# Optimization experiments

Hardware: AMD Instinct MI355X
Metric: run time of the kernel (lower is better)

The kernel has to match this reference:

```python
import jax, jax.numpy as jnp
import numpy as np
import math

D_MODEL = 1024
NUM_HEADS = 16
HEAD_DIM = D_MODEL // NUM_HEADS
THETA = 10000.0
B, S = 2, 2048


def _rope(x, positions, theta):
    # x: (b, h, s, d); positions: (s,) int
    d = x.shape[-1]
    inv_freq = theta ** (-jnp.arange(0, d, 2, dtype=jnp.float32) / d)  # (d/2,)
    ang = positions.astype(jnp.float32)[:, None] * inv_freq[None, :]   # (s, d/2)
    cos, sin = jnp.cos(ang), jnp.sin(ang)
    x1 = x[..., ::2]
    x2 = x[..., 1::2]
    r1 = x1 * cos - x2 * sin
    r2 = x1 * sin + x2 * cos
    # interleave back to (..., d)
    return jnp.stack([r1, r2], axis=-1).reshape(x.shape)


def setup_inputs() -> dict:
    key = jax.random.key(0)
    ks = jax.random.split(key, 5)
    std = math.sqrt(2.0 / (D_MODEL + D_MODEL))
    return {
        "x": jax.random.normal(ks[0], (B, S, D_MODEL), dtype=jnp.float32),
        "token_positions": jnp.arange(S, dtype=jnp.int32),
        "Wq": jax.random.normal(ks[1], (D_MODEL, D_MODEL), dtype=jnp.float32) * std,
        "Wk": jax.random.normal(ks[2], (D_MODEL, D_MODEL), dtype=jnp.float32) * std,
        "Wv": jax.random.normal(ks[3], (D_MODEL, D_MODEL), dtype=jnp.float32) * std,
        "Wo": jax.random.normal(ks[4], (D_MODEL, D_MODEL), dtype=jnp.float32) * std,
    }


def reference(x, token_positions, Wq, Wk, Wv, Wo):
    b, s, _ = x.shape
    def split_heads(t):
        return t.reshape(b, s, NUM_HEADS, HEAD_DIM).transpose(0, 2, 1, 3)  # (b,h,s,d)
    Q = split_heads(x @ Wq.T)
    K = split_heads(x @ Wk.T)
    V = split_heads(x @ Wv.T)
    Q = _rope(Q, token_positions, THETA)
    K = _rope(K, token_positions, THETA)
    scores = jnp.einsum("bhqd,bhkd->bhqk", Q, K) / math.sqrt(HEAD_DIM)
    causal = jnp.tril(jnp.ones((s, s), dtype=bool))
    scores = jnp.where(causal, scores, -jnp.inf)
    attn = jax.nn.softmax(scores, axis=-1)
    out = jnp.einsum("bhqk,bhkd->bhqd", attn, V)
    out = out.transpose(0, 2, 1, 3).reshape(b, s, D_MODEL)
    return out @ Wo.T
```

## Files before the change

kernel.cpp:

```cpp
#include <hip/hip_runtime.h>
#include <math.h>

typedef unsigned short u16;
typedef unsigned int   u32;
typedef __attribute__((ext_vector_type(8))) short bf16x8;
typedef __attribute__((ext_vector_type(4))) float floatx4;
typedef __attribute__((ext_vector_type(4))) _Float16 halfx4;
typedef __attribute__((ext_vector_type(2))) unsigned int uintx2;

#define SEQ 2048
#define DM  1024
#define NH  16
#define DH  64
#define MM  4096
#define QSCALE 0.18033688011112042f

__device__ __forceinline__ u16 f2bf(float f) {
    u32 u = __builtin_bit_cast(u32, f);
    u += 0x7fffu + ((u >> 16) & 1u);
    return (u16)(u >> 16);
}

__device__ __forceinline__ void async16(const void* g, void* l) {
    __builtin_amdgcn_global_load_lds(
        (const __attribute__((address_space(1))) void*)g,
        (__attribute__((address_space(3))) void*)l, 16, 0, 0);
}

__global__ __launch_bounds__(256) void prep_kernel(const float* __restrict__ x,
                                                   const float* __restrict__ w0,
                                                   const float* __restrict__ w1,
                                                   const float* __restrict__ w2,
                                                   const float* __restrict__ w3,
                                                   u16* __restrict__ Xsh,
                                                   u16* __restrict__ Wsh,
                                                   const int* __restrict__ pos,
                                                   float2* __restrict__ tab) {
    const int bid = blockIdx.x, cb = blockIdx.y, tid = threadIdx.x;

    int lin = bid * 16 + cb;
    if (lin < 256) {
        int i = lin * 256 + tid;
        int p = i >> 5, d2 = i & 31;
        float freq = __expf(-(float)d2 * (9.2103403719761836f / 32.0f));
        float sv, cv;
        sincosf((float)pos[p] * freq, &sv, &cv);
        tab[i] = make_float2(cv, sv);
    }

    const float* src; u16* dst; int row0;
    if (bid < 64) { src = x; dst = Xsh; row0 = bid * 64; }
    else {
        int wi = (bid - 64) >> 4;
        src = (wi == 0) ? w0 : (wi == 1) ? w1 : (wi == 2) ? w2 : w3;
        dst = Wsh + (size_t)wi * DM * DM;
        row0 = ((bid - 64) & 15) * 64;
    }
    __shared__ __align__(16) u16 t[64 * 64];
#pragma unroll
    for (int rep = 0; rep < 4; ++rep) {
        int f = rep * 256 + tid;
        int r = f >> 4, c4 = f & 15;
        float4 v = *(const float4*)&src[(size_t)(row0 + r) * DM + cb * 64 + c4 * 4];
        uint2 pk;
        pk.x = (u32)f2bf(v.x) | ((u32)f2bf(v.y) << 16);
        pk.y = (u32)f2bf(v.z) | ((u32)f2bf(v.w) << 16);
        int ch = (c4 >> 1) ^ (r & 7);
        *(uint2*)&t[r * 64 + ch * 8 + (c4 & 1) * 4] = pk;
    }
    __syncthreads();
#pragma unroll
    for (int rep = 0; rep < 2; ++rep) {
        int s = rep * 256 + tid;
        int tile = s >> 6, l = s & 63;
        int mt = tile >> 1, kt = tile & 1, lm = l & 15, quad = l >> 4;
        int m = mt * 16 + lm;
        uint4 v = *(const uint4*)&t[m * 64 + ((kt * 4 + quad) ^ (m & 7)) * 8];
        size_t rowblk = (size_t)(row0 >> 4) + mt;
        size_t ktile  = cb * 2 + kt;
        *(uint4*)&dst[(rowblk * 32 + ktile) * 512 + l * 8] = v;
    }
}

template<int NZ, bool OUTF32>
__global__ __launch_bounds__(256, 2) void gemm_f(const u16* __restrict__ Ash,
                                                 const u16* __restrict__ Wbase,
                                                 u16* __restrict__ outbf,
                                                 float* __restrict__ outf,
                                                 _Float16* __restrict__ vtout,
                                                 const float2* __restrict__ ropetab) {
    const int m0 = blockIdx.x * 64, n0 = blockIdx.y * 128;
    const int tid = threadIdx.x, lane = tid & 63, w = tid >> 6;
    const int lm = lane & 15, quad = lane >> 4;
    const int rb0 = m0 >> 4;
    const int cb0 = n0 >> 4;

    __shared__ __align__(16) u16 lsA[2][4 * 512];
    __shared__ __align__(16) u16 lsB[2][NZ * 8 * 512];

    const u16* aSrc = Ash + ((size_t)(rb0 + w) * 32) * 512 + lane * 8;
    constexpr int NPW = NZ * 2;
    const u16* bSrc[NPW];
#pragma unroll
    for (int j = 0; j < NPW; ++j) {
        int p = w * NPW + j, z = p >> 3, cb8 = p & 7;
        bSrc[j] = Wbase + (size_t)z * (DM * DM)
                + ((size_t)(cb0 + cb8) * 32) * 512 + lane * 8;
    }

    auto stage = [&](int buf, int it) {
        async16(aSrc + (size_t)it * 512, &lsA[buf][w * 512 + lane * 8]);
#pragma unroll
        for (int j = 0; j < NPW; ++j)
            async16(bSrc[j] + (size_t)it * 512,
                    &lsB[buf][(w * NPW + j) * 512 + lane * 8]);
    };

    floatx4 acc[NZ][4][2];
    const floatx4 z4 = {0.f, 0.f, 0.f, 0.f};
#pragma unroll
    for (int z = 0; z < NZ; ++z)
#pragma unroll
        for (int mt = 0; mt < 4; ++mt)
#pragma unroll
            for (int nt = 0; nt < 2; ++nt) acc[z][mt][nt] = z4;

    stage(0, 0);
    __syncthreads();

#pragma unroll 2
    for (int it = 0; it < 32; ++it) {
        if (it < 31) stage((it + 1) & 1, it + 1);
        const u16* La = &lsA[it & 1][0];
        const u16* Lb = &lsB[it & 1][0];
        bf16x8 a[4], b[NZ][2];
#pragma unroll
        for (int mt = 0; mt < 4; ++mt)
            a[mt] = *(const bf16x8*)&La[mt * 512 + lane * 8];
#pragma unroll
        for (int z = 0; z < NZ; ++z)
#pragma unroll
            for (int nt = 0; nt < 2; ++nt)
                b[z][nt] = *(const bf16x8*)&Lb[(z * 8 + w * 2 + nt) * 512 + lane * 8];
#pragma unroll
        for (int z = 0; z < NZ; ++z)
#pragma unroll
            for (int mt = 0; mt < 4; ++mt)
#pragma unroll
                for (int nt = 0; nt < 2; ++nt)
                    acc[z][mt][nt] = __builtin_amdgcn_mfma_f32_16x16x32_bf16(
                        a[mt], b[z][nt], acc[z][mt][nt], 0, 0, 0);
        __syncthreads();
    }

#pragma unroll
    for (int z = 0; z < NZ; ++z) {
        if (!OUTF32 && NZ == 3 && z == 2) {
#pragma unroll
            for (int mt = 0; mt < 4; ++mt) {
                int row = m0 + mt * 16 + quad * 4;
                int b = row >> 11, s = row & (SEQ - 1);
#pragma unroll
                for (int nt = 0; nt < 2; ++nt) {
                    int col = n0 + w * 32 + nt * 16 + lm;
                    uint2 pk;
                    pk.x = __builtin_bit_cast(u32, __builtin_amdgcn_cvt_pkrtz(acc[z][mt][nt][0], acc[z][mt][nt][1]));
                    pk.y = __builtin_bit_cast(u32, __builtin_amdgcn_cvt_pkrtz(acc[z][mt][nt][2], acc[z][mt][nt][3]));
                    *(uint2*)&vtout[((size_t)b * NH * DH + (size_t)col) * SEQ + s] = pk;
                }
            }
            continue;
        }
        const bool rope = !OUTF32;
        const float osc = (!OUTF32 && z == 0) ? QSCALE : 1.0f;
#pragma unroll
        for (int mt = 0; mt < 4; ++mt)
#pragma unroll
            for (int r = 0; r < 4; ++r) {
                int row = m0 + mt * 16 + quad * 4 + r;
#pragma unroll
                for (int nt = 0; nt < 2; ++nt) {
                    int col = n0 + w * 32 + nt * 16 + lm;
                    float v  = acc[z][mt][nt][r];
                    if (rope) {
                        float pv = __shfl_xor(v, 1);
                        float2 cs = ropetab[(row & (SEQ - 1)) * 32 + ((col & 63) >> 1)];
                        v = (lm & 1) ? fmaf(pv, cs.y, v * cs.x) : fmaf(v, cs.x, -pv * cs.y);
                    }
                    v *= osc;
                    if (OUTF32) {
                        outf[(size_t)row * DM + col] = v;
                    } else {
                        float hv = __shfl_xor(v, 1);
                        if (!(lm & 1)) {
                            u32 pk = (u32)f2bf(v) | ((u32)f2bf(hv) << 16);
                            *(u32*)&outbf[(size_t)z * ((size_t)MM * DM) + (size_t)row * DM + col] = pk;
                        }
                    }
                }
            }
    }
}

__global__ __launch_bounds__(256, 2) void attn_kernel(const u16* __restrict__ Q,
                                                      const u16* __restrict__ K,
                                                      const _Float16* __restrict__ Vt,
                                                      u16* __restrict__ AO) {
    const int u  = blockIdx.x;
    const int qt = (u < 256) ? (15 - (u >> 5)) : ((u >> 5) - 8);
    const int bh = u & 31;
    const int b  = bh >> 4, h = bh & 15;
    const int q0 = qt * 128;
    const int tid = threadIdx.x, w = tid >> 6, lane = tid & 63;
    const int lm = lane & 15, quad = lane >> 4;

    __shared__ __align__(16) u16      lsK[2][128 * 64];
    __shared__ __align__(16) _Float16 lsV[2][64 * 128];

    bf16x8 qb[2][2];
#pragma unroll
    for (int qi = 0; qi < 2; ++qi)
#pragma unroll
        for (int ks = 0; ks < 2; ++ks)
            qb[qi][ks] = *(const bf16x8*)
                &Q[(size_t)(b * SEQ + q0 + w * 32 + qi * 16 + lm) * DM + h * DH + ks * 32 + quad * 8];

    const floatx4 z4 = {0.f, 0.f, 0.f, 0.f};
    floatx4 o[2][4];
#pragma unroll
    for (int qi = 0; qi < 2; ++qi)
#pragma unroll
        for (int dt = 0; dt < 4; ++dt) o[qi][dt] = z4;
    float lsum[2] = {0.f, 0.f};

    auto stageKV = [&](int buf, int kt) {
#pragma unroll
        for (int rep = 0; rep < 4; ++rep) {
            int f = rep * 256 + tid;
            int krow = f >> 3, kcb = (f & 7) ^ (krow & 7);
            async16(&K[(size_t)(b * SEQ + kt * 128 + krow) * DM + h * DH + kcb * 8],
                    &lsK[buf][f * 8]);
            int d = f >> 4, gbs = (f & 15) ^ ((d >> 1) & 7);
            async16(&Vt[(size_t)(bh * DH + d) * SEQ + kt * 128 + gbs * 8],
                    &lsV[buf][f * 8]);
        }
    };

    stageKV(0, 0);
    for (int kt = 0; kt <= qt; ++kt) {
        __syncthreads();
        if (kt < qt) stageKV((kt + 1) & 1, kt + 1);
        const u16*      Lk = lsK[kt & 1];
        const _Float16* Lv = lsV[kt & 1];

        floatx4 s4[2][8];
#pragma unroll
        for (int qi = 0; qi < 2; ++qi)
#pragma unroll
            for (int st = 0; st < 8; ++st) s4[qi][st] = z4;
#pragma unroll
        for (int ks = 0; ks < 2; ++ks) {
            const int cbl = ((ks * 4 + quad) ^ (lm & 7)) * 8;
#pragma unroll
            for (int st = 0; st < 8; ++st) {
                bf16x8 ka = *(const bf16x8*)&Lk[(st * 16 + lm) * 64 + cbl];
#pragma unroll
                for (int qi = 0; qi < 2; ++qi)
                    s4[qi][st] = __builtin_amdgcn_mfma_f32_16x16x32_bf16(ka, qb[qi][ks], s4[qi][st], 0, 0, 0);
            }
        }

        const bool diag = (kt == qt);
#pragma unroll
        for (int st = 0; st < 8; ++st) {
            halfx4 pb2[2];
#pragma unroll
            for (int qi = 0; qi < 2; ++qi) {
#pragma unroll
                for (int r = 0; r < 4; ++r) {
                    float v = s4[qi][st][r];
                    if (diag) {
                        int keyloc = st * 16 + quad * 4 + r;
                        if (keyloc > w * 32 + qi * 16 + lm) v = -1e30f;
                    }
                    v = exp2f(v);
                    lsum[qi] += v;
                    s4[qi][st][r] = v;
                }
                uintx2 pk2;
                pk2.x = __builtin_bit_cast(u32, __builtin_amdgcn_cvt_pkrtz(s4[qi][st][0], s4[qi][st][1]));
                pk2.y = __builtin_bit_cast(u32, __builtin_amdgcn_cvt_pkrtz(s4[qi][st][2], s4[qi][st][3]));
                pb2[qi] = __builtin_bit_cast(halfx4, pk2);
            }
#pragma unroll
            for (int dt = 0; dt < 4; ++dt) {
                int drow = dt * 16 + lm;
                int sbs = (st * 2 + (quad >> 1)) ^ ((drow >> 1) & 7);
                halfx4 va = *(const halfx4*)&Lv[drow * 128 + sbs * 8 + (quad & 1) * 4];
#pragma unroll
                for (int qi = 0; qi < 2; ++qi)
                    o[qi][dt] = __builtin_amdgcn_mfma_f32_16x16x16f16(va, pb2[qi], o[qi][dt], 0, 0, 0);
            }
        }
    }

    float rl[2];
#pragma unroll
    for (int qi = 0; qi < 2; ++qi) {
        lsum[qi] += __shfl_xor(lsum[qi], 16);
        lsum[qi] += __shfl_xor(lsum[qi], 32);
        rl[qi] = 1.0f / lsum[qi];
    }

    __syncthreads();
    u16* eb = (u16*)&lsK[0][0];
#pragma unroll
    for (int qi = 0; qi < 2; ++qi) {
        const int q = w * 32 + qi * 16 + lm;
#pragma unroll
        for (int dt = 0; dt < 4; ++dt) {
            uint2 pk;
            pk.x = (u32)f2bf(o[qi][dt][0] * rl[qi]) | ((u32)f2bf(o[qi][dt][1] * rl[qi]) << 16);
            pk.y = (u32)f2bf(o[qi][dt][2] * rl[qi]) | ((u32)f2bf(o[qi][dt][3] * rl[qi]) << 16);
            int ch = (dt * 2 + (quad >> 1)) ^ (lm & 7);
            *(uint2*)&eb[q * 64 + ch * 8 + (quad & 1) * 4] = pk;
        }
    }
    __syncthreads();
    const size_t rowblk0 = (size_t)((b * SEQ + q0) >> 4);
#pragma unroll
    for (int rbi = 0; rbi < 2; ++rbi) {
#pragma unroll
        for (int kt = 0; kt < 2; ++kt) {
            uint4 v = *(const uint4*)&eb[((w * 2 + rbi) * 16 + lm) * 64 + ((kt * 4 + quad) ^ (lm & 7)) * 8];
            *(uint4*)&AO[((rowblk0 + w * 2 + rbi) * 32 + (h * 2 + kt)) * 512 + lane * 8] = v;
        }
    }
}

extern "C" void kernel_launch(void* const* d_in, const int* in_sizes, int n_in,
                              void* d_out, int out_size, void* d_ws, size_t ws_size,
                              hipStream_t stream) {
    const float* x   = (const float*)d_in[0];
    const int*   pos = (const int*)d_in[1];
    float* out = (float*)d_out;

    u16* ws = (u16*)d_ws;
    const size_t MD = (size_t)MM * DM;
    const size_t DD = (size_t)DM * DM;
    u16* Xsh = ws;
    u16* Wsh = ws + MD;
    u16* Qbf = ws + MD + 4 * DD;
    u16* Kbf = Qbf + MD;
    u16* VtB = Kbf + MD;
    float2* ropetab = (float2*)(VtB + MD);
    _Float16* Vt = (_Float16*)VtB;
    u16* AOsh = Xsh;

    prep_kernel<<<dim3(128, 16), 256, 0, stream>>>(
        x, (const float*)d_in[2], (const float*)d_in[3], (const float*)d_in[4],
        (const float*)d_in[5], Xsh, Wsh, pos, ropetab);

    gemm_f<3, false><<<dim3(64, 8), 256, 0, stream>>>(
        Xsh, Wsh, Qbf, nullptr, Vt, ropetab);

    attn_kernel<<<dim3(512), 256, 0, stream>>>(Qbf, Kbf, Vt, AOsh);

    gemm_f<1, true><<<dim3(64, 8), 256, 0, stream>>>(
        AOsh, Wsh + 3 * DD, nullptr, out, nullptr, ropetab);
}
```

Measured before the change: 187.3 us.

## Store V in MFMA fragment order, halve KV tile, compute row sums via MFMA

The QKV projection now writes V in a chunked layout that matches the attention MFMA operand fragments, so V tiles load into LDS with contiguous copies and no swizzle. The attention loop moves to 64-key tiles with half-size LDS buffers and raises the occupancy target in launch bounds from 2 to 4 blocks. K is staged directly in fragment order. The softmax denominator is produced by an extra MFMA against a ones vector instead of scalar adds and cross-lane shuffles. This trades more loop iterations and barriers, plus one extra MFMA per step, for higher occupancy, simpler addressing and fewer VALU instructions.

```diff
diff --git a/kernel.cpp b/kernel.cpp
--- a/kernel.cpp
+++ b/kernel.cpp
@@ -158,15 +158,19 @@
         if (!OUTF32 && NZ == 3 && z == 2) {
 #pragma unroll
             for (int mt = 0; mt < 4; ++mt) {
-                int row = m0 + mt * 16 + quad * 4;
-                int b = row >> 11, s = row & (SEQ - 1);
+                int row = m0 + mt * 16;
+                int b = row >> 11;
+                int sblk = (row & (SEQ - 1)) >> 4;
 #pragma unroll
                 for (int nt = 0; nt < 2; ++nt) {
-                    int col = n0 + w * 32 + nt * 16 + lm;
+                    int col = n0 + w * 32 + nt * 16;
+                    int h = col >> 6;
+                    int dblk = (col & 63) >> 4;
+                    size_t chunk = ((size_t)(b * NH + h) * 128 + sblk) * 4 + dblk;
                     uint2 pk;
                     pk.x = __builtin_bit_cast(u32, __builtin_amdgcn_cvt_pkrtz(acc[z][mt][nt][0], acc[z][mt][nt][1]));
                     pk.y = __builtin_bit_cast(u32, __builtin_amdgcn_cvt_pkrtz(acc[z][mt][nt][2], acc[z][mt][nt][3]));
-                    *(uint2*)&vtout[((size_t)b * NH * DH + (size_t)col) * SEQ + s] = pk;
+                    *(uint2*)&vtout[chunk * 256 + lane * 4] = pk;
                 }
             }
             continue;
@@ -202,9 +206,9 @@
     }
 }
 
-__global__ __launch_bounds__(256, 2) void attn_kernel(const u16* __restrict__ Q,
+__global__ __launch_bounds__(256, 4) void attn_kernel(const u16* __restrict__ Q,
                                                       const u16* __restrict__ K,
-                                                      const _Float16* __restrict__ Vt,
+                                                      const _Float16* __restrict__ Vf,
                                                       u16* __restrict__ AO) {
     const int u  = blockIdx.x;
     const int qt = (u < 256) ? (15 - (u >> 5)) : ((u >> 5) - 8);
@@ -214,8 +218,8 @@
     const int tid = threadIdx.x, w = tid >> 6, lane = tid & 63;
     const int lm = lane & 15, quad = lane >> 4;
 
-    __shared__ __align__(16) u16      lsK[2][128 * 64];
-    __shared__ __align__(16) _Float16 lsV[2][64 * 128];
+    __shared__ __align__(16) u16      lsK[2][8 * 512];
+    __shared__ __align__(16) _Float16 lsV[2][16 * 256];
 
     bf16x8 qb[2][2];
 #pragma unroll
@@ -227,65 +231,70 @@
 
     const floatx4 z4 = {0.f, 0.f, 0.f, 0.f};
     floatx4 o[2][4];
-#pragma unroll
-    for (int qi = 0; qi < 2; ++qi)
+    floatx4 o5[2];
+#pragma unroll
+    for (int qi = 0; qi < 2; ++qi) {
 #pragma unroll
         for (int dt = 0; dt < 4; ++dt) o[qi][dt] = z4;
-    float lsum[2] = {0.f, 0.f};
+        o5[qi] = z4;
+    }
+
+    const u16* Kb = K + (size_t)(b * SEQ) * DM + h * DH + (size_t)lm * DM + quad * 8;
+    const _Float16* Vb = Vf + (size_t)bh * (128 * 4 * 256);
 
     auto stageKV = [&](int buf, int kt) {
 #pragma unroll
-        for (int rep = 0; rep < 4; ++rep) {
-            int f = rep * 256 + tid;
-            int krow = f >> 3, kcb = (f & 7) ^ (krow & 7);
-            async16(&K[(size_t)(b * SEQ + kt * 128 + krow) * DM + h * DH + kcb * 8],
-                    &lsK[buf][f * 8]);
-            int d = f >> 4, gbs = (f & 15) ^ ((d >> 1) & 7);
-            async16(&Vt[(size_t)(bh * DH + d) * SEQ + kt * 128 + gbs * 8],
-                    &lsV[buf][f * 8]);
+        for (int j = 0; j < 2; ++j) {
+            int c = w * 2 + j;
+            async16(Kb + (size_t)(kt * 64 + (c >> 1) * 16) * DM + (c & 1) * 32,
+                    &lsK[buf][c * 512 + lane * 8]);
+        }
+#pragma unroll
+        for (int p = 0; p < 2; ++p) {
+            int off = p * 2048 + w * 512 + lane * 8;
+            async16(Vb + (size_t)kt * 4096 + off, &lsV[buf][off]);
         }
     };
 
     stageKV(0, 0);
-    for (int kt = 0; kt <= qt; ++kt) {
+    const int nkt = 2 * qt + 2;
+    const halfx4 ones = {(_Float16)1.f, (_Float16)1.f, (_Float16)1.f, (_Float16)1.f};
+
+    for (int kt = 0; kt < nkt; ++kt) {
         __syncthreads();
-        if (kt < qt) stageKV((kt + 1) & 1, kt + 1);
+        if (kt + 1 < nkt) stageKV((kt + 1) & 1, kt + 1);
         const u16*      Lk = lsK[kt & 1];
         const _Float16* Lv = lsV[kt & 1];
 
-        floatx4 s4[2][8];
+        floatx4 s4[2][4];
 #pragma unroll
         for (int qi = 0; qi < 2; ++qi)
 #pragma unroll
-            for (int st = 0; st < 8; ++st) s4[qi][st] = z4;
-#pragma unroll
-        for (int ks = 0; ks < 2; ++ks) {
-            const int cbl = ((ks * 4 + quad) ^ (lm & 7)) * 8;
-#pragma unroll
-            for (int st = 0; st < 8; ++st) {
-                bf16x8 ka = *(const bf16x8*)&Lk[(st * 16 + lm) * 64 + cbl];
+            for (int st = 0; st < 4; ++st) s4[qi][st] = z4;
+#pragma unroll
+        for (int ks = 0; ks < 2; ++ks)
+#pragma unroll
+            for (int st = 0; st < 4; ++st) {
+                bf16x8 ka = *(const bf16x8*)&Lk[(st * 2 + ks) * 512 + lane * 8];
 #pragma unroll
                 for (int qi = 0; qi < 2; ++qi)
                     s4[qi][st] = __builtin_amdgcn_mfma_f32_16x16x32_bf16(ka, qb[qi][ks], s4[qi][st], 0, 0, 0);
             }
-        }
-
-        const bool diag = (kt == qt);
-#pragma unroll
-        for (int st = 0; st < 8; ++st) {
+
+        const int rel = kt - 2 * qt;
+#pragma unroll
+        for (int st = 0; st < 4; ++st) {
             halfx4 pb2[2];
 #pragma unroll
             for (int qi = 0; qi < 2; ++qi) {
 #pragma unroll
                 for (int r = 0; r < 4; ++r) {
                     float v = s4[qi][st][r];
-                    if (diag) {
-                        int keyloc = st * 16 + quad * 4 + r;
+                    if (rel >= 0) {
+                        int keyloc = rel * 64 + st * 16 + quad * 4 + r;
                         if (keyloc > w * 32 + qi * 16 + lm) v = -1e30f;
                     }
-                    v = exp2f(v);
-                    lsum[qi] += v;
-                    s4[qi][st][r] = v;
+                    s4[qi][st][r] = exp2f(v);
                 }
                 uintx2 pk2;
                 pk2.x = __builtin_bit_cast(u32, __builtin_amdgcn_cvt_pkrtz(s4[qi][st][0], s4[qi][st][1]));
@@ -294,23 +303,18 @@
             }
 #pragma unroll
             for (int dt = 0; dt < 4; ++dt) {
-                int drow = dt * 16 + lm;
-                int sbs = (st * 2 + (quad >> 1)) ^ ((drow >> 1) & 7);
-                halfx4 va = *(const halfx4*)&Lv[drow * 128 + sbs * 8 + (quad & 1) * 4];
+                halfx4 va = *(const halfx4*)&Lv[(st * 4 + dt) * 256 + lane * 4];
 #pragma unroll
                 for (int qi = 0; qi < 2; ++qi)
                     o[qi][dt] = __builtin_amdgcn_mfma_f32_16x16x16f16(va, pb2[qi], o[qi][dt], 0, 0, 0);
             }
-        }
-    }
-
-    float rl[2];
-#pragma unroll
-    for (int qi = 0; qi < 2; ++qi) {
-        lsum[qi] += __shfl_xor(lsum[qi], 16);
-        lsum[qi] += __shfl_xor(lsum[qi], 32);
-        rl[qi] = 1.0f / lsum[qi];
-    }
+#pragma unroll
+            for (int qi = 0; qi < 2; ++qi)
+                o5[qi] = __builtin_amdgcn_mfma_f32_16x16x16f16(ones, pb2[qi], o5[qi], 0, 0, 0);
+        }
+    }
+
+    float rl[2] = {1.0f / o5[0][0], 1.0f / o5[1][0]};
 
     __syncthreads();
     u16* eb = (u16*)&lsK[0][0];
```

After: 207.0 us. 10.5% more time.
